# Kernel tuning notes

Measured on AMD Instinct MI355X. Metric: run time of the kernel, lower is better.

Reference implementation:

```python
import jax, jax.numpy as jnp
import numpy as np

N = 50000          # nodes
E = 1_600_000      # edges
R = 16             # num_relations
NB = 4             # num_bases
FIN = 128          # num_node_features
H = 128            # hidden_channels
G = 64             # num graphs in batch
NC = 2             # num_classes


def rgcn_conv(x, edge_index, edge_type, bases, comp, root, bias):
    """PyG RGCNConv with basis decomposition, mean aggregation per relation."""
    n = x.shape[0]
    # weight[r] = sum_b comp[r,b] * bases[b]  -> [R, in, out]
    weight = jnp.einsum('rb,bio->rio', comp, bases)
    src, dst = edge_index[0], edge_index[1]
    # segment id combining destination node and relation
    seg = dst * R + edge_type                      # [E]
    msg = x[src]                                   # [E, in] gather
    summed = jax.ops.segment_sum(msg, seg, num_segments=n * R)      # [N*R, in]
    cnt = jax.ops.segment_sum(jnp.ones((msg.shape[0],), x.dtype), seg,
                              num_segments=n * R)                   # [N*R]
    mean = summed / jnp.maximum(cnt, 1.0)[:, None]
    mean = mean.reshape(n, R, -1)                  # [N, R, in]
    out = jnp.einsum('nri,rio->no', mean, weight) + x @ root + bias
    return out


def global_mean_pool(x, batch, num_graphs):
    s = jax.ops.segment_sum(x, batch, num_segments=num_graphs)
    c = jax.ops.segment_sum(jnp.ones((x.shape[0],), x.dtype), batch,
                            num_segments=num_graphs)
    return s / jnp.maximum(c, 1.0)[:, None]


def setup_inputs() -> dict:
    key = jax.random.key(0)
    ks = jax.random.split(key, 24)
    inp = {
        'x': jax.random.normal(ks[0], (N, FIN), jnp.float32),
        'edge_index': jax.random.randint(ks[1], (2, E), 0, N),
        'edge_type': jax.random.randint(ks[2], (E,), 0, R),
        'batch': jnp.sort(jax.random.randint(ks[3], (N,), 0, G)),
        'rel_labels': jax.random.randint(ks[4], (G,), 0, R),
        'drop_prob': 0,
        'rel_emb': jax.random.normal(ks[5], (R, H), jnp.float32),
    }
    s1 = 1.0 / np.sqrt(FIN)
    s2 = 1.0 / np.sqrt(H)
    inp['bases1'] = jax.random.normal(ks[6], (NB, FIN, H), jnp.float32) * s1
    inp['comp1'] = jax.random.normal(ks[7], (R, NB), jnp.float32)
    inp['root1'] = jax.random.normal(ks[8], (FIN, H), jnp.float32) * s1
    inp['bias1'] = jnp.zeros((H,), jnp.float32)
    inp['bases2'] = jax.random.normal(ks[9], (NB, H, H), jnp.float32) * s2
    inp['comp2'] = jax.random.normal(ks[10], (R, NB), jnp.float32)
    inp['root2'] = jax.random.normal(ks[11], (H, H), jnp.float32) * s2
    inp['bias2'] = jnp.zeros((H,), jnp.float32)
    inp['bases3'] = jax.random.normal(ks[12], (NB, H, H), jnp.float32) * s2
    inp['comp3'] = jax.random.normal(ks[13], (R, NB), jnp.float32)
    inp['root3'] = jax.random.normal(ks[14], (H, H), jnp.float32) * s2
    inp['bias3'] = jnp.zeros((H,), jnp.float32)
    inp['lin_w'] = jax.random.normal(ks[15], (2 * H, NC), jnp.float32) * (1.0 / np.sqrt(2 * H))
    inp['lin_b'] = jnp.zeros((NC,), jnp.float32)
    return inp


def reference(x, edge_index, edge_type, batch, rel_labels, drop_prob, rel_emb,
              bases1, comp1, root1, bias1,
              bases2, comp2, root2, bias2,
              bases3, comp3, root3, bias3,
              lin_w, lin_b):
    rel_embs = rel_emb[rel_labels]                               # [G, H]
    h = jax.nn.relu(rgcn_conv(x, edge_index, edge_type, bases1, comp1, root1, bias1))
    h = jax.nn.relu(rgcn_conv(h, edge_index, edge_type, bases2, comp2, root2, bias2))
    h = rgcn_conv(h, edge_index, edge_type, bases3, comp3, root3, bias3)
    pooled = global_mean_pool(h, batch, G)                       # [G, H]
    z = jnp.concatenate([pooled, rel_embs], axis=1)              # [G, 2H]
    # dropout with p=drop_prob in eval mode (reference is deterministic) -> identity
    return z @ lin_w + lin_b                                     # [G, NC]
```

## Files before the change

kernel.cpp:

```cpp
#include <hip/hip_runtime.h>

#define NN 50000
#define EE 1600000
#define RR 16
#define NBASE 4
#define FINF 128
#define HD 128
#define NG 64
#define NCLS 2
#define NRSEG (NN*RR)

typedef __attribute__((ext_vector_type(8))) short short8;
typedef __attribute__((ext_vector_type(4))) float f32x4;
typedef __attribute__((ext_vector_type(2))) float f32x2;
typedef unsigned short u16;
typedef unsigned int u32;
typedef unsigned long long u64;
typedef unsigned char u8;

__device__ __forceinline__ float bflo(u32 u){ return __builtin_bit_cast(float, u << 16); }
__device__ __forceinline__ float bfhi(u32 u){ return __builtin_bit_cast(float, u & 0xFFFF0000u); }
__device__ __forceinline__ u16 f2bf(float f){
  u32 u = __builtin_bit_cast(u32, f);
  u += 0x7FFFu + ((u >> 16) & 1u);
  return (u16)(u >> 16);
}
__device__ __forceinline__ u32 pack2(float a, float b){
  return (u32)f2bf(a) | ((u32)f2bf(b) << 16);
}
__device__ __forceinline__ u32 cvt_pk_bf16(float a, float b){
  u32 r;
  asm("v_cvt_pk_bf16_f32 %0, %1, %2" : "=v"(r) : "v"(a), "v"(b));
  return r;
}
__device__ __forceinline__ float fastrcp(float x){
#if __has_builtin(__builtin_amdgcn_rcpf)
  return __builtin_amdgcn_rcpf(x);
#else
  return 1.0f / x;
#endif
}
__device__ __forceinline__ float ldf(const void* p, int i, int isbf){
  return isbf ? bflo((u32)((const u16*)p)[i]) : ((const float*)p)[i];
}

__device__ __forceinline__ float fp8_manual(u32 b){
  u32 s = (b>>7)&1, e = (b>>3)&15, m = b&7;
  float v;
  if (e==0) v = (float)m * 0.001953125f;
  else      v = __builtin_bit_cast(float, ((e+120u)<<23) | (m<<20));
  return s ? -v : v;
}
__device__ __forceinline__ u32 f32_to_fp8_manual(float f){
  u32 u = __builtin_bit_cast(u32, f);
  u32 s = u>>31;
  int e = (int)((u>>23)&0xFF);
  u32 m = u & 0x7FFFFF;
  int ee = e - 120;
  if (ee <= 0) return s<<7;
  u32 m3 = m >> 20, rem = m & 0xFFFFF;
  u32 rnd = (rem > 0x80000u) || (rem == 0x80000u && (m3 & 1));
  m3 += rnd;
  if (m3 == 8){ m3 = 0; ee += 1; }
  if (ee >= 16){ ee = 15; m3 = 6; }
  return (s<<7) | ((u32)ee<<3) | m3;
}
__device__ __forceinline__ void fp8x2_to_f32(u32 v, float& a, float& b){
#if __has_builtin(__builtin_amdgcn_cvt_pk_f32_fp8)
  f32x2 r = __builtin_amdgcn_cvt_pk_f32_fp8((int)v, false);
  a = r[0]; b = r[1];
#else
  a = fp8_manual(v & 0xFF); b = fp8_manual((v>>8)&0xFF);
#endif
}
__device__ __forceinline__ u32 pk_fp8x2(float a, float b){
  a = fminf(fmaxf(a, -448.f), 448.f);
  b = fminf(fmaxf(b, -448.f), 448.f);
#if __has_builtin(__builtin_amdgcn_cvt_pk_fp8_f32)
  return (u32)__builtin_amdgcn_cvt_pk_fp8_f32(a, b, 0, false) & 0xFFFF;
#else
  return f32_to_fp8_manual(a) | (f32_to_fp8_manual(b) << 8);
#endif
}

__global__ void k_detect(const u32* __restrict__ xw, int* __restrict__ flag){
  __shared__ int votes;
  if (threadIdx.x == 0) votes = 0;
  __syncthreads();
  u32 w = xw[threadIdx.x];
  int e = (w >> 7) & 0xFF;
  if (e >= 100 && e <= 129) atomicAdd(&votes, 1);
  __syncthreads();
  if (threadIdx.x == 0) flag[0] = (votes >= 192) ? 1 : 0;
}

__global__ void k_quant(const void* __restrict__ src, u8* __restrict__ dstq,
                        const int* __restrict__ flagp, int* __restrict__ cnt){
  int i = blockIdx.x*256 + threadIdx.x;
  if (i < NRSEG) cnt[i] = 0;
  if (i >= NN*HD/4) return;
  int isbf = flagp[0];
  float v0,v1,v2,v3;
  if (isbf){
    u32 a = ((const u32*)src)[i*2+0], b = ((const u32*)src)[i*2+1];
    v0=bflo(a); v1=bfhi(a); v2=bflo(b); v3=bfhi(b);
  } else {
    float4 f = ((const float4*)src)[i];
    v0=f.x; v1=f.y; v2=f.z; v3=f.w;
  }
  u32 q = pk_fp8x2(v0,v1) | (pk_fp8x2(v2,v3) << 16);
  ((u32*)dstq)[i] = q;
}


__global__ void k_hist(const int* __restrict__ dst, const int* __restrict__ et,
                       int* __restrict__ cnt){
  int e = blockIdx.x*256 + threadIdx.x;
  if (e < EE) atomicAdd(&cnt[et[e]*NN + dst[e]], 1);
}

#define SCB 1024
__global__ __launch_bounds__(SCB) void k_scan1(const int* __restrict__ cnt,
                                               int* __restrict__ off,
                                               int* __restrict__ bsum){
  __shared__ int sh[SCB];
  int tid = threadIdx.x;
  int i = blockIdx.x*SCB + tid;
  int v = (i < NRSEG) ? cnt[i] : 0;
  sh[tid] = v; __syncthreads();
  for (int d=1; d<SCB; d<<=1){
    int t = (tid >= d) ? sh[tid-d] : 0;
    __syncthreads();
    sh[tid] += t;
    __syncthreads();
  }
  if (i < NRSEG) off[i] = sh[tid] - v;
  if (tid == SCB-1) bsum[blockIdx.x] = sh[SCB-1];
}

__global__ __launch_bounds__(1024) void k_scan2(int* __restrict__ bsum, int nb){
  __shared__ int sh[1024];
  __shared__ int carry;
  int tid = threadIdx.x;
  if (tid == 0) carry = 0;
  __syncthreads();
  for (int base=0; base<nb; base+=1024){
    int i = base + tid;
    int v = (i < nb) ? bsum[i] : 0;
    int orig = v;
    sh[tid] = v; __syncthreads();
    for (int d=1; d<1024; d<<=1){
      int t = (tid >= d) ? sh[tid-d] : 0;
      __syncthreads();
      sh[tid] += t;
      __syncthreads();
    }
    int total = sh[1023];
    int excl = sh[tid] - orig + carry;
    if (i < nb) bsum[i] = excl;
    __syncthreads();
    if (tid == 0) carry += total;
    __syncthreads();
  }
}

__global__ __launch_bounds__(SCB) void k_scan3(const int* __restrict__ cnt,
                                               int* __restrict__ off,
                                               const int* __restrict__ bsum){
  int i = blockIdx.x*SCB + threadIdx.x;
  if (i < NRSEG){
    int o = off[i] + bsum[blockIdx.x];
    off[i] = o;
    if (i == NRSEG-1) off[NRSEG] = o + cnt[i];
  }
}

__global__ void k_scatter(const int* __restrict__ src, const int* __restrict__ dst,
                          const int* __restrict__ et, const int* __restrict__ off,
                          int* __restrict__ cnt, int* __restrict__ esrc){
  int e = blockIdx.x*256 + threadIdx.x;
  if (e < EE){
    int seg = et[e]*NN + dst[e];
    int p = atomicSub(&cnt[seg], 1) - 1;
    esrc[off[seg] + p] = src[e] << 7;
  }
}


__global__ void k_weights3(const void* __restrict__ b0, const void* __restrict__ c0,
                           const void* __restrict__ r0,
                           const void* __restrict__ b1, const void* __restrict__ c1,
                           const void* __restrict__ r1,
                           const void* __restrict__ b2, const void* __restrict__ c2,
                           const void* __restrict__ r2,
                           u16* __restrict__ WTf, const int* __restrict__ flagp){
  int gid = blockIdx.x;
  int layer = gid / 1088;
  int blk = gid - layer*1088;
  int idx = blk*256 + threadIdx.x;
  if (idx >= 17*16384) return;
  const void* bases = (layer==0) ? b0 : (layer==1) ? b1 : b2;
  const void* comp  = (layer==0) ? c0 : (layer==1) ? c1 : c2;
  const void* root  = (layer==0) ? r0 : (layer==1) ? r1 : r2;
  u16* W = WTf + (u32)layer * (17*16384);
  int isbf = flagp[0];
  int r = idx >> 14;
  int o = (idx >> 7) & 127;
  int i = idx & 127;
  float v;
  if (r < RR){
    v = 0.f;
    #pragma unroll
    for (int b=0;b<NBASE;b++)
      v += ldf(comp, r*NBASE+b, isbf) * ldf(bases, (b*FINF + i)*HD + o, isbf);
  } else {
    v = ldf(root, i*HD + o, isbf);
  }
  int wv = o >> 5, ct = (o >> 4) & 1, mrow = o & 15;
  int ks = i >> 5, quad = (i >> 3) & 3, j = i & 7;
  int lane = quad*16 + mrow;
  W[(u32)((((r*4+wv)*2+ct)*4+ks)*64 + lane)*8 + j] = f2bf(v);
}


#define TN 16

#define GLD(rg, ei) { u32 voff_ = (u32)__builtin_amdgcn_readlane(eiv, (ei)) + lane2u; \
  asm volatile("global_load_ushort %0, %1, %2" : "=v"(rg) : "v"(voff_), "s"(xq)); }
#define WAITV0 { asm volatile("s_waitcnt vmcnt(0)" ::: "memory"); \
  __builtin_amdgcn_sched_barrier(0); }
#define CNS(rg, k) if ((k) < cnt){ int eg_ = sbeg + (k); \
  while (idx < TN && nbv <= eg_) doflush(); \
  float da_, db_; fp8x2_to_f32(rg, da_, db_); a0 += da_; a1 += db_; }

__global__ __launch_bounds__(256, 6) void k_layer(
    const u8*  __restrict__ xq,
    const u16* __restrict__ WTf,
    const void* __restrict__ bias, const int* __restrict__ off,
    const int* __restrict__ esrc,
    u16* __restrict__ hout,
    u8* __restrict__ hq,
    const int* __restrict__ flagp, int write_bf, int relu)
{
  __shared__ __align__(16) u16 Abuf[4][TN*136];
  __shared__ int soff[RR*17];
  int tid = threadIdx.x;
  int n0 = blockIdx.x * TN;
  int isbf_in = flagp[0];

  int wv = tid >> 6;
  int lane = tid & 63;
  u32 lane2u = (u32)(lane << 1);
  int mrow = lane & 15;
  int quad = lane >> 4;

  for (int i = tid; i < RR*17; i += 256){
    int r = i / 17, k = i - r*17;
    soff[i] = off[r*NN + n0 + k];
  }
  __syncthreads();

  f32x4 acc[2];
  { f32x4 z = {0.f,0.f,0.f,0.f}; acc[0] = z; acc[1] = z; }

  for (int t=0; t<4; ++t){
    int r = t*4 + wv;
    {
      int offv = 0;
      if (lane <= 16) offv = soff[r*17 + lane];
      int wstart = __builtin_amdgcn_readlane(offv, 0);
      int wend   = __builtin_amdgcn_readlane(offv, 16);
      int blen = wend - wstart;

      float a0 = 0.f, a1 = 0.f;
      int idx = 0;
      int cb = wstart;
      int nbv = __builtin_amdgcn_readlane(offv, 1);
      u16* abase = Abuf[wv] + lane*2;

      auto doflush = [&](){
        int cnt_ = nbv - cb;
        float cf = (float)(cnt_ > 0 ? cnt_ : 1);
        float inv = fastrcp(cf);
        *(u32*)(abase + idx*136) = cvt_pk_bf16(a0*inv, a1*inv);
        a0 = 0.f; a1 = 0.f;
        cb = nbv; idx++;
        if (idx < TN) nbv = __builtin_amdgcn_readlane(offv, idx+1);
      };

      if (blen > 0 && blen <= 128){
        int c0 = blen - 1;
        int eiv0 = esrc[wstart + (lane < c0 ? lane : c0)];
        int eiv1 = 0;
        if (blen > 64){
          int c1 = blen - 65;
          eiv1 = esrc[wstart + 64 + (lane < c1 ? lane : c1)];
        }

        auto batch32 = [&](int eiv, int lb, int sbeg, int cnt)
            __attribute__((always_inline)) {
          u32 r0,r1,r2,r3,r4,r5,r6,r7,r8,r9,r10,r11,r12,r13,r14,r15,
              r16,r17,r18,r19,r20,r21,r22,r23,r24,r25,r26,r27,r28,r29,r30,r31;
          GLD(r0, lb+0) GLD(r1, lb+1) GLD(r2, lb+2) GLD(r3, lb+3)
          GLD(r4, lb+4) GLD(r5, lb+5) GLD(r6, lb+6) GLD(r7, lb+7)
          if (cnt > 8){
            GLD(r8, lb+8)  GLD(r9, lb+9)  GLD(r10, lb+10) GLD(r11, lb+11)
            GLD(r12, lb+12) GLD(r13, lb+13) GLD(r14, lb+14) GLD(r15, lb+15)
          }
          if (cnt > 16){
            GLD(r16, lb+16) GLD(r17, lb+17) GLD(r18, lb+18) GLD(r19, lb+19)
            GLD(r20, lb+20) GLD(r21, lb+21) GLD(r22, lb+22) GLD(r23, lb+23)
          }
          if (cnt > 24){
            GLD(r24, lb+24) GLD(r25, lb+25) GLD(r26, lb+26) GLD(r27, lb+27)
            GLD(r28, lb+28) GLD(r29, lb+29) GLD(r30, lb+30) GLD(r31, lb+31)
          }
          WAITV0
          CNS(r0, 0) CNS(r1, 1) CNS(r2, 2) CNS(r3, 3)
          CNS(r4, 4) CNS(r5, 5) CNS(r6, 6) CNS(r7, 7)
          CNS(r8, 8) CNS(r9, 9) CNS(r10, 10) CNS(r11, 11)
          CNS(r12, 12) CNS(r13, 13) CNS(r14, 14) CNS(r15, 15)
          CNS(r16, 16) CNS(r17, 17) CNS(r18, 18) CNS(r19, 19)
          CNS(r20, 20) CNS(r21, 21) CNS(r22, 22) CNS(r23, 23)
          CNS(r24, 24) CNS(r25, 25) CNS(r26, 26) CNS(r27, 27)
          CNS(r28, 28) CNS(r29, 29) CNS(r30, 30) CNS(r31, 31)
        };

        int cnt0 = blen < 64 ? blen : 64;
        int cA = cnt0 < 32 ? cnt0 : 32;
        batch32(eiv0, 0, wstart, cA);
        if (cnt0 > 32) batch32(eiv0, 32, wstart + 32, cnt0 - 32);
        if (blen > 64){
          int cnt1 = blen - 64;
          int cB = cnt1 < 32 ? cnt1 : 32;
          batch32(eiv1, 0, wstart + 64, cB);
          if (cnt1 > 32) batch32(eiv1, 32, wstart + 96, cnt1 - 32);
        }
      } else if (blen > 0){
        for (int e = wstart; e < wend; ++e){
          int sid = __builtin_amdgcn_readfirstlane(esrc[e]);
          while (idx < TN && nbv <= e) doflush();
          float da, db;
          fp8x2_to_f32((u32)*(const u16*)(xq + (u32)sid + lane2u), da, db);
          a0 += da; a1 += db;
        }
      }
      while (idx < TN) doflush();
    }
    __syncthreads();
    #pragma unroll
    for (int rloc=0; rloc<4; ++rloc){
      int rr = t*4 + rloc;
      const u16* Bp = WTf + (u32)(((rr*4 + wv)*2)*4*64)*8 + (u32)lane*8;
      #pragma unroll
      for (int ks=0; ks<4; ++ks){
        short8 af = *(const short8*)(Abuf[rloc] + mrow*136 + ks*32 + quad*8);
        #pragma unroll
        for (int ct=0; ct<2; ++ct){
          short8 bf = *(const short8*)(Bp + (u32)(ct*4 + ks)*64*8);
          acc[ct] = __builtin_amdgcn_mfma_f32_16x16x32_bf16(af, bf, acc[ct], 0, 0, 0);
        }
      }
    }
    __syncthreads();
  }
  {
    const u8* xrow = xq + (u32)(n0 + mrow)*HD;
    const u16* Bp = WTf + (u32)(((16*4 + wv)*2)*4*64)*8 + (u32)lane*8;
    #pragma unroll
    for (int ks=0; ks<4; ++ks){
      u32 lo = *(const u32*)(xrow + ks*32 + quad*8);
      u32 hi = *(const u32*)(xrow + ks*32 + quad*8 + 4);
      float f0,f1,f2,f3,f4,f5,f6,f7;
      fp8x2_to_f32(lo & 0xFFFFu, f0, f1);
      fp8x2_to_f32(lo >> 16,     f2, f3);
      fp8x2_to_f32(hi & 0xFFFFu, f4, f5);
      fp8x2_to_f32(hi >> 16,     f6, f7);
      union { short8 v; u32 w[4]; } u;
      u.w[0] = cvt_pk_bf16(f0,f1); u.w[1] = cvt_pk_bf16(f2,f3);
      u.w[2] = cvt_pk_bf16(f4,f5); u.w[3] = cvt_pk_bf16(f6,f7);
      #pragma unroll
      for (int ct=0; ct<2; ++ct){
        short8 bf = *(const short8*)(Bp + (u32)(ct*4 + ks)*64*8);
        acc[ct] = __builtin_amdgcn_mfma_f32_16x16x32_bf16(u.v, bf, acc[ct], 0, 0, 0);
      }
    }
  }
  #pragma unroll
  for (int ct=0; ct<2; ++ct){
    int col = wv*32 + ct*16 + mrow;
    float bv = ldf(bias, col, isbf_in);
    #pragma unroll
    for (int rg=0; rg<4; ++rg){
      int n = n0 + quad*4 + rg;
      float v = acc[ct][rg] + bv;
      if (relu) v = fmaxf(v, 0.f);
      if (!(v == v)) v = 0.f;
      if (write_bf) hout[(u32)(n*HD + col)] = f2bf(v);
      else          hq[(u32)(n*HD + col)] = (u8)(pk_fp8x2(v, 0.f) & 0xFF);
    }
  }
}


__global__ __launch_bounds__(1024) void k_pool_head(
    const u16* __restrict__ h, const int* __restrict__ batch,
    const int* __restrict__ rlab, const void* __restrict__ rel_emb,
    const void* __restrict__ lin_w, const void* __restrict__ lin_b,
    void* __restrict__ out, const int* __restrict__ flagp)
{
  int g = blockIdx.x;
  int isbf = flagp[0];
  __shared__ int bounds[2];
  __shared__ float psum[8][128];
  __shared__ float red[4];
  if (threadIdx.x == 0){
    int lo=0, hi=NN;
    while (lo < hi){ int m=(lo+hi)>>1; if (batch[m] < g) lo=m+1; else hi=m; }
    bounds[0] = lo;
    int lo2=lo, hi2=NN;
    while (lo2 < hi2){ int m=(lo2+hi2)>>1; if (batch[m] < g+1) lo2=m+1; else hi2=m; }
    bounds[1] = lo2;
  }
  __syncthreads();
  int lo = bounds[0], hi = bounds[1];
  int f = threadIdx.x & 127;
  int s = threadIdx.x >> 7;
  float acc = 0.f;
  for (int n = lo + s; n < hi; n += 8) acc += bflo((u32)h[(u32)(n*HD + f)]);
  psum[s][f] = acc;
  __syncthreads();
  if (threadIdx.x < 128){
    int cn = hi - lo;
    float tot = 0.f;
    #pragma unroll
    for (int k=0;k<8;k++) tot += psum[k][f];
    float pooled = tot / (float)(cn > 0 ? cn : 1);
    int rl = rlab[g];
    float re = ldf(rel_emb, rl*HD + f, isbf);
    float v0 = pooled * ldf(lin_w, f*NCLS+0, isbf) + re * ldf(lin_w, (HD+f)*NCLS+0, isbf);
    float v1 = pooled * ldf(lin_w, f*NCLS+1, isbf) + re * ldf(lin_w, (HD+f)*NCLS+1, isbf);
    #pragma unroll
    for (int o=32;o>0;o>>=1){ v0 += __shfl_down(v0,o); v1 += __shfl_down(v1,o); }
    int ln = threadIdx.x & 63, wvv = threadIdx.x >> 6;
    if (ln == 0){ red[wvv*2] = v0; red[wvv*2+1] = v1; }
  }
  __syncthreads();
  if (threadIdx.x == 0){
    float o0 = red[0] + red[2] + ldf(lin_b, 0, isbf);
    float o1 = red[1] + red[3] + ldf(lin_b, 1, isbf);
    if (isbf){
      ((u16*)out)[g*NCLS+0] = f2bf(o0);
      ((u16*)out)[g*NCLS+1] = f2bf(o1);
    } else {
      ((float*)out)[g*NCLS+0] = o0;
      ((float*)out)[g*NCLS+1] = o1;
    }
  }
}


extern "C" void kernel_launch(void* const* d_in, const int* in_sizes, int n_in,
                              void* d_out, int out_size, void* d_ws, size_t ws_size,
                              hipStream_t stream)
{
  (void)in_sizes; (void)n_in; (void)out_size; (void)ws_size;
  const void* x      = d_in[0];
  const int* eidx    = (const int*)d_in[1];
  const int* etype   = (const int*)d_in[2];
  const int* batch   = (const int*)d_in[3];
  const int* rlab    = (const int*)d_in[4];
  const void* rel_emb = d_in[6];
  const void* basesA[3] = {d_in[7],  d_in[11], d_in[15]};
  const void* compA[3]  = {d_in[8],  d_in[12], d_in[16]};
  const void* rootA[3]  = {d_in[9],  d_in[13], d_in[17]};
  const void* biasA[3]  = {d_in[10], d_in[14], d_in[18]};
  const void* lin_w  = d_in[19];
  const void* lin_b  = d_in[20];

  char* p = (char*)d_ws;
  auto alloc = [&](size_t bytes)->char*{ char* r = p; p += (bytes + 255) & ~(size_t)255; return r; };
  int*   flag   = (int*)  alloc(256);
  int*   off    = (int*)  alloc((size_t)(NRSEG+1)*4);
  int*   esrc   = (int*)  alloc((size_t)(EE+64)*4);
  u16*   WTf    = (u16*)  alloc((size_t)3*17*16384*2);
  u8*    xq     = (u8*)   alloc((size_t)NN*HD);
  u8*    h1q    = (u8*)   alloc((size_t)NN*HD);
  u8*    h2q    = (u8*)   alloc((size_t)NN*HD);
  u16*   h3     = (u16*)  alloc((size_t)NN*HD*2);
  int*   cnt    = (int*)h3;
  int*   bsum   = (int*)((char*)h3 + (size_t)NRSEG*4);

  const int* src_in = eidx;
  const int* dst_in = eidx + EE;

  const int nscan = (NRSEG + SCB - 1) / SCB;

  k_detect <<<1, 256, 0, stream>>>((const u32*)x, flag);
  k_quant  <<<(NN*HD/4 + 255)/256, 256, 0, stream>>>(x, xq, flag, cnt);
  k_hist   <<<EE/256, 256, 0, stream>>>(dst_in, etype, cnt);
  k_scan1  <<<nscan, SCB, 0, stream>>>(cnt, off, bsum);
  k_scan2  <<<1,    1024, 0, stream>>>(bsum, nscan);
  k_scan3  <<<nscan, SCB, 0, stream>>>(cnt, off, bsum);
  k_scatter<<<EE/256, 256, 0, stream>>>(src_in, dst_in, etype, off, cnt, esrc);

  k_weights3<<<3*1088, 256, 0, stream>>>(basesA[0], compA[0], rootA[0],
                                         basesA[1], compA[1], rootA[1],
                                         basesA[2], compA[2], rootA[2],
                                         WTf, flag);

  const int nblk = NN / TN;
  u16* W0 = WTf;
  u16* W1 = WTf + (size_t)1*17*16384;
  u16* W2 = WTf + (size_t)2*17*16384;
  k_layer<<<nblk, 256, 0, stream>>>(xq,  W0, biasA[0], off, esrc, (u16*)0, h1q, flag, 0, 1);
  k_layer<<<nblk, 256, 0, stream>>>(h1q, W1, biasA[1], off, esrc, (u16*)0, h2q, flag, 0, 1);
  k_layer<<<nblk, 256, 0, stream>>>(h2q, W2, biasA[2], off, esrc, h3, (u8*)0, flag, 1, 0);

  k_pool_head<<<NG, 1024, 0, stream>>>(h3, batch, rlab, rel_emb, lin_w, lin_b,
                                       d_out, flag);
}
```

Measured before the change: 608.8 us.

## Double node tile per block and reuse weight fragments across two M-tiles

Raises the per-block node tile from 16 to 32. Each wave now loads its B-fragment weights into registers once and applies them to two 16-row MFMA tiles, halving weight reloads per node in both the relation and root GEMMs. The occupancy hint drops from 6 to 4 blocks per CU to allow the larger accumulator and fragment register set. A ragged last block is handled by clamping offsets and guarding stores, but the root-term feature reads for the padded rows are unguarded and can run past the end of the input.

```diff
diff --git a/kernel.cpp b/kernel.cpp
--- a/kernel.cpp
+++ b/kernel.cpp
@@ -24,9 +24,6 @@
   u32 u = __builtin_bit_cast(u32, f);
   u += 0x7FFFu + ((u >> 16) & 1u);
   return (u16)(u >> 16);
-}
-__device__ __forceinline__ u32 pack2(float a, float b){
-  return (u32)f2bf(a) | ((u32)f2bf(b) << 16);
 }
 __device__ __forceinline__ u32 cvt_pk_bf16(float a, float b){
   u32 r;
@@ -223,7 +220,7 @@
 }
 
 
-#define TN 16
+#define TN 32
 
 #define GLD(rg, ei) { u32 voff_ = (u32)__builtin_amdgcn_readlane(eiv, (ei)) + lane2u; \
   asm volatile("global_load_ushort %0, %1, %2" : "=v"(rg) : "v"(voff_), "s"(xq)); }
@@ -233,7 +230,7 @@
   while (idx < TN && nbv <= eg_) doflush(); \
   float da_, db_; fp8x2_to_f32(rg, da_, db_); a0 += da_; a1 += db_; }
 
-__global__ __launch_bounds__(256, 6) void k_layer(
+__global__ __launch_bounds__(256, 4) void k_layer(
     const u8*  __restrict__ xq,
     const u16* __restrict__ WTf,
     const void* __restrict__ bias, const int* __restrict__ off,
@@ -243,7 +240,7 @@
     const int* __restrict__ flagp, int write_bf, int relu)
 {
   __shared__ __align__(16) u16 Abuf[4][TN*136];
-  __shared__ int soff[RR*17];
+  __shared__ int soff[RR*(TN+1)];
   int tid = threadIdx.x;
   int n0 = blockIdx.x * TN;
   int isbf_in = flagp[0];
@@ -254,22 +251,24 @@
   int mrow = lane & 15;
   int quad = lane >> 4;
 
-  for (int i = tid; i < RR*17; i += 256){
-    int r = i / 17, k = i - r*17;
-    soff[i] = off[r*NN + n0 + k];
-  }
-  __syncthreads();
-
-  f32x4 acc[2];
-  { f32x4 z = {0.f,0.f,0.f,0.f}; acc[0] = z; acc[1] = z; }
+  for (int i = tid; i < RR*(TN+1); i += 256){
+    int r = i / (TN+1), k = i - r*(TN+1);
+    int n = n0 + k; if (n > NN) n = NN;
+    soff[i] = off[r*NN + n];
+  }
+  __syncthreads();
+
+  f32x4 acc[2][2];
+  { f32x4 z = {0.f,0.f,0.f,0.f};
+    acc[0][0]=z; acc[0][1]=z; acc[1][0]=z; acc[1][1]=z; }
 
   for (int t=0; t<4; ++t){
     int r = t*4 + wv;
     {
       int offv = 0;
-      if (lane <= 16) offv = soff[r*17 + lane];
+      if (lane <= TN) offv = soff[r*(TN+1) + lane];
       int wstart = __builtin_amdgcn_readlane(offv, 0);
-      int wend   = __builtin_amdgcn_readlane(offv, 16);
+      int wend   = __builtin_amdgcn_readlane(offv, TN);
       int blen = wend - wstart;
 
       float a0 = 0.f, a1 = 0.f;
@@ -352,52 +351,71 @@
     for (int rloc=0; rloc<4; ++rloc){
       int rr = t*4 + rloc;
       const u16* Bp = WTf + (u32)(((rr*4 + wv)*2)*4*64)*8 + (u32)lane*8;
+      short8 bf[2][4];
       #pragma unroll
-      for (int ks=0; ks<4; ++ks){
-        short8 af = *(const short8*)(Abuf[rloc] + mrow*136 + ks*32 + quad*8);
+      for (int ct=0; ct<2; ++ct)
         #pragma unroll
-        for (int ct=0; ct<2; ++ct){
-          short8 bf = *(const short8*)(Bp + (u32)(ct*4 + ks)*64*8);
-          acc[ct] = __builtin_amdgcn_mfma_f32_16x16x32_bf16(af, bf, acc[ct], 0, 0, 0);
+        for (int ks=0; ks<4; ++ks)
+          bf[ct][ks] = *(const short8*)(Bp + (u32)(ct*4 + ks)*64*8);
+      #pragma unroll
+      for (int mt=0; mt<2; ++mt){
+        #pragma unroll
+        for (int ks=0; ks<4; ++ks){
+          short8 af = *(const short8*)(Abuf[rloc] + (mt*16 + mrow)*136 + ks*32 + quad*8);
+          #pragma unroll
+          for (int ct=0; ct<2; ++ct)
+            acc[mt][ct] = __builtin_amdgcn_mfma_f32_16x16x32_bf16(af, bf[ct][ks], acc[mt][ct], 0, 0, 0);
         }
       }
     }
     __syncthreads();
   }
   {
-    const u8* xrow = xq + (u32)(n0 + mrow)*HD;
     const u16* Bp = WTf + (u32)(((16*4 + wv)*2)*4*64)*8 + (u32)lane*8;
-    #pragma unroll
-    for (int ks=0; ks<4; ++ks){
-      u32 lo = *(const u32*)(xrow + ks*32 + quad*8);
-      u32 hi = *(const u32*)(xrow + ks*32 + quad*8 + 4);
-      float f0,f1,f2,f3,f4,f5,f6,f7;
-      fp8x2_to_f32(lo & 0xFFFFu, f0, f1);
-      fp8x2_to_f32(lo >> 16,     f2, f3);
-      fp8x2_to_f32(hi & 0xFFFFu, f4, f5);
-      fp8x2_to_f32(hi >> 16,     f6, f7);
-      union { short8 v; u32 w[4]; } u;
-      u.w[0] = cvt_pk_bf16(f0,f1); u.w[1] = cvt_pk_bf16(f2,f3);
-      u.w[2] = cvt_pk_bf16(f4,f5); u.w[3] = cvt_pk_bf16(f6,f7);
+    short8 bf[2][4];
+    #pragma unroll
+    for (int ct=0; ct<2; ++ct)
       #pragma unroll
-      for (int ct=0; ct<2; ++ct){
-        short8 bf = *(const short8*)(Bp + (u32)(ct*4 + ks)*64*8);
-        acc[ct] = __builtin_amdgcn_mfma_f32_16x16x32_bf16(u.v, bf, acc[ct], 0, 0, 0);
+      for (int ks=0; ks<4; ++ks)
+        bf[ct][ks] = *(const short8*)(Bp + (u32)(ct*4 + ks)*64*8);
+    #pragma unroll
+    for (int mt=0; mt<2; ++mt){
+      const u8* xrow = xq + (u32)(n0 + mt*16 + mrow)*HD;
+      #pragma unroll
+      for (int ks=0; ks<4; ++ks){
+        u32 lo = *(const u32*)(xrow + ks*32 + quad*8);
+        u32 hi = *(const u32*)(xrow + ks*32 + quad*8 + 4);
+        float f0,f1,f2,f3,f4,f5,f6,f7;
+        fp8x2_to_f32(lo & 0xFFFFu, f0, f1);
+        fp8x2_to_f32(lo >> 16,     f2, f3);
+        fp8x2_to_f32(hi & 0xFFFFu, f4, f5);
+        fp8x2_to_f32(hi >> 16,     f6, f7);
+        union { short8 v; u32 w[4]; } u;
+        u.w[0] = cvt_pk_bf16(f0,f1); u.w[1] = cvt_pk_bf16(f2,f3);
+        u.w[2] = cvt_pk_bf16(f4,f5); u.w[3] = cvt_pk_bf16(f6,f7);
+        #pragma unroll
+        for (int ct=0; ct<2; ++ct)
+          acc[mt][ct] = __builtin_amdgcn_mfma_f32_16x16x32_bf16(u.v, bf[ct][ks], acc[mt][ct], 0, 0, 0);
       }
     }
   }
   #pragma unroll
-  for (int ct=0; ct<2; ++ct){
-    int col = wv*32 + ct*16 + mrow;
-    float bv = ldf(bias, col, isbf_in);
-    #pragma unroll
-    for (int rg=0; rg<4; ++rg){
-      int n = n0 + quad*4 + rg;
-      float v = acc[ct][rg] + bv;
-      if (relu) v = fmaxf(v, 0.f);
-      if (!(v == v)) v = 0.f;
-      if (write_bf) hout[(u32)(n*HD + col)] = f2bf(v);
-      else          hq[(u32)(n*HD + col)] = (u8)(pk_fp8x2(v, 0.f) & 0xFF);
+  for (int mt=0; mt<2; ++mt){
+    #pragma unroll
+    for (int ct=0; ct<2; ++ct){
+      int col = wv*32 + ct*16 + mrow;
+      float bv = ldf(bias, col, isbf_in);
+      #pragma unroll
+      for (int rg=0; rg<4; ++rg){
+        int n = n0 + mt*16 + quad*4 + rg;
+        if (n < NN){
+          float v = acc[mt][ct][rg] + bv;
+          if (relu) v = fmaxf(v, 0.f);
+          if (!(v == v)) v = 0.f;
+          if (write_bf) hout[(u32)(n*HD + col)] = f2bf(v);
+          else          hq[(u32)(n*HD + col)] = (u8)(pk_fp8x2(v, 0.f) & 0xFF);
+        }
+      }
     }
   }
 }
@@ -509,7 +527,7 @@
                                          basesA[2], compA[2], rootA[2],
                                          WTf, flag);
 
-  const int nblk = NN / TN;
+  const int nblk = (NN + TN - 1) / TN;
   u16* W0 = WTf;
   u16* W1 = WTf + (size_t)1*17*16384;
   u16* W2 = WTf + (size_t)2*17*16384;
```

After: 660.8 us. 8.5% more time.
